# Kernel optimization log

Measured on AMD Instinct MI355X. Metric: run time of the kernel, lower is better.

The kernel has to match this reference:

```python
import jax, jax.numpy as jnp
import numpy as np

FP_PENALTY = 1.0  # false_positive_penalty from __init__ (missing_penalty is unused in forward)


def setup_inputs() -> dict:
    key = jax.random.key(0)
    k1, k2, k3 = jax.random.split(key, 3)
    B, C, H, W = 8, 9, 512, 512
    T = 16  # targets per image
    policy_output = jax.random.normal(k1, (B, C, H, W), dtype=jnp.float32)
    target_boxes = jax.random.randint(k2, (B, T, 4), 0, 512, dtype=jnp.int32)
    target_probs = jax.random.uniform(k3, (B, T), dtype=jnp.float32)
    return {"policy_output": policy_output, "target_boxes": target_boxes,
            "target_probs": target_probs}


def reference(policy_output, target_boxes, target_probs):
    B, C, H, W = policy_output.shape
    A = 3
    T = target_boxes.shape[1]

    out = policy_output.reshape(B, A, 3, H, W)
    delta_r = jax.nn.sigmoid(out[:, :, 0]) * 9.0    # (B,A,H,W)
    delta_c = jax.nn.sigmoid(out[:, :, 1]) * 16.0   # (B,A,H,W)
    conf = jax.nn.sigmoid(out[:, :, 2])             # (B,A,H,W)

    r_grid = jnp.arange(H, dtype=jnp.float32)[None, None, :, None]  # (1,1,H,1)
    c_grid = jnp.arange(W, dtype=jnp.float32)[None, None, None, :]  # (1,1,1,W)
    pred_r2 = jnp.clip(r_grid + delta_r, 0.0, H - 1.0)  # (B,A,H,W)
    pred_c2 = jnp.clip(c_grid + delta_c, 0.0, W - 1.0)  # (B,A,H,W)
    pr2_i = jnp.round(pred_r2).astype(jnp.int32)
    pc2_i = jnp.round(pred_c2).astype(jnp.int32)

    r_i = jnp.arange(H, dtype=jnp.int32)[None, None, :, None, None]  # (1,1,H,1,1)
    c_i = jnp.arange(W, dtype=jnp.int32)[None, None, None, :, None]  # (1,1,1,W,1)
    tb = target_boxes[:, None, None, None, :, :]  # (B,1,1,1,T,4)

    # match iff (r==tr1 and c==tc1 and round(pred_r2)==tr2 and round(pred_c2)==tc2)
    match = ((r_i == tb[..., 0]) & (c_i == tb[..., 1]) &
             (pr2_i[..., None] == tb[..., 2]) & (pc2_i[..., None] == tb[..., 3]))  # (B,A,H,W,T)
    has_match = match.any(-1)                 # (B,A,H,W)
    first_idx = jnp.argmax(match, axis=-1)    # first matching target (torch loop breaks)

    gather = jax.vmap(lambda v, i: v[i])      # per-batch gather along T
    tr2 = gather(target_boxes[:, :, 2].astype(jnp.float32), first_idx)  # (B,A,H,W)
    tc2 = gather(target_boxes[:, :, 3].astype(jnp.float32), first_idx)
    tp = gather(target_probs, first_idx)

    coord_loss = jnp.abs(pred_r2 - tr2) + jnp.abs(pred_c2 - tc2)
    conf_loss = (conf - tp) ** 2
    fp_loss = conf ** 2 * FP_PENALTY

    per_anchor = jnp.where(has_match, coord_loss + conf_loss, fp_loss)
    denom = max(1, B * H * W * 3)
    return per_anchor.sum() / denom
```

## Files before the change

kernel.cpp:

```cpp
#include <hip/hip_runtime.h>


#define NB 1024
#define NT 256

__device__ __forceinline__ float sigmoidf_(float x) {
    float e = __builtin_amdgcn_exp2f(-1.4426950408889634f * x);
    return 1.0f / (1.0f + e);
}

__global__ __launch_bounds__(NT) void conf_sum_kernel(const float* __restrict__ pol,
                                                      float* __restrict__ partials) {
    const int tid = threadIdx.x;
    const int gid = blockIdx.x * NT + tid;
    const float4* p4 = (const float4*)pol;
    float acc = 0.f;
#pragma unroll
    for (int it = 0; it < 6; ++it) {
        int i = gid + it * (NB * NT);
        int plane = i >> 16;
        int off = i & 65535;
        int b = plane / 3;
        int a = plane - 3 * b;
        int chan = b * 9 + a * 3 + 2;
        float4 v = p4[((size_t)chan << 16) + off];
        float s0 = sigmoidf_(v.x);
        float s1 = sigmoidf_(v.y);
        float s2 = sigmoidf_(v.z);
        float s3 = sigmoidf_(v.w);
        acc += s0 * s0 + s1 * s1 + s2 * s2 + s3 * s3;
    }
#pragma unroll
    for (int o = 32; o; o >>= 1) acc += __shfl_down(acc, o);
    __shared__ float sw[NT / 64];
    if ((tid & 63) == 0) sw[tid >> 6] = acc;
    __syncthreads();
    if (tid == 0) partials[blockIdx.x] = sw[0] + sw[1] + sw[2] + sw[3];
}

__global__ __launch_bounds__(NT) void finish_kernel(const float* __restrict__ pol,
                                                    const int* __restrict__ tb,
                                                    const float* __restrict__ tp,
                                                    const float* __restrict__ partials,
                                                    float* __restrict__ out) {
    const int tid = threadIdx.x;
    double acc = 0.0;

    for (int it = tid; it < 384; it += NT) {
        int a = it % 3;
        int bt = it / 3;
        int t = bt & 15;
        int b = bt >> 4;
        const int* tbb = tb + b * 64;
        int r = tbb[t * 4 + 0];
        int c = tbb[t * 4 + 1];
        bool dup = false;
        for (int t2 = 0; t2 < t; ++t2)
            if (tbb[t2 * 4 + 0] == r && tbb[t2 * 4 + 1] == c) { dup = true; break; }
        if (dup) continue;

        size_t base = ((size_t)(b * 9 + a * 3)) << 18;
        size_t pix = ((size_t)r << 9) + (size_t)c;
        float x0 = pol[base + pix];
        float x1 = pol[base + (1 << 18) + pix];
        float x2 = pol[base + (2 << 18) + pix];
        float dr = sigmoidf_(x0) * 9.0f;
        float dc = sigmoidf_(x1) * 16.0f;
        float conf = sigmoidf_(x2);
        float pr2 = fminf((float)r + dr, 511.0f);
        float pc2 = fminf((float)c + dc, 511.0f);
        int pr2i = (int)rintf(pr2);
        int pc2i = (int)rintf(pc2);

        int fidx = -1;
        for (int t2 = 0; t2 < 16; ++t2) {
            if (tbb[t2 * 4 + 0] == r && tbb[t2 * 4 + 1] == c &&
                tbb[t2 * 4 + 2] == pr2i && tbb[t2 * 4 + 3] == pc2i) { fidx = t2; break; }
        }
        if (fidx >= 0) {
            float tr2 = (float)tbb[fidx * 4 + 2];
            float tc2 = (float)tbb[fidx * 4 + 3];
            float tpv = tp[b * 16 + fidx];
            float coord = fabsf(pr2 - tr2) + fabsf(pc2 - tc2);
            float closs = (conf - tpv) * (conf - tpv);
            acc += (double)(coord + closs - conf * conf);
        }
    }

    for (int j = tid; j < NB; j += NT) acc += (double)partials[j];

#pragma unroll
    for (int o = 32; o; o >>= 1) acc += __shfl_down(acc, o);
    __shared__ double sd[NT / 64];
    if ((tid & 63) == 0) sd[tid >> 6] = acc;
    __syncthreads();
    if (tid == 0) {
        double total = sd[0] + sd[1] + sd[2] + sd[3];
        out[0] = (float)(total / 6291456.0);
    }
}

extern "C" void kernel_launch(void* const* d_in, const int* in_sizes, int n_in,
                              void* d_out, int out_size, void* d_ws, size_t ws_size,
                              hipStream_t stream) {
    const float* pol = (const float*)d_in[0];
    const int* tb = (const int*)d_in[1];
    const float* tp = (const float*)d_in[2];
    float* partials = (float*)d_ws;
    float* out = (float*)d_out;

    conf_sum_kernel<<<NB, NT, 0, stream>>>(pol, partials);
    finish_kernel<<<1, NT, 0, stream>>>(pol, tb, tp, partials, out);
}
```

Baseline: 115.6 us.

## Fuse conf-sum and finish kernels using last-block atomic counter reduction

Merges the two launches into one grid of NB+1 blocks. The extra block computes the matched-anchor correction in parallel with the conf-sum blocks. The last block to finish, found through an atomic counter, does the final double-precision reduction. This removes the serial single-block second kernel launch but adds a memset of the counter on every call. The matched-anchor partial is now accumulated in float instead of double.

```diff
diff --git a/kernel.cpp b/kernel.cpp
--- a/kernel.cpp
+++ b/kernel.cpp
@@ -9,94 +9,101 @@
     return 1.0f / (1.0f + e);
 }
 
-__global__ __launch_bounds__(NT) void conf_sum_kernel(const float* __restrict__ pol,
-                                                      float* __restrict__ partials) {
+__global__ __launch_bounds__(NT) void fused_kernel(const float* __restrict__ pol,
+                                                   const int* __restrict__ tb,
+                                                   const float* __restrict__ tp,
+                                                   float* __restrict__ partials,
+                                                   unsigned int* __restrict__ counter,
+                                                   float* __restrict__ out) {
     const int tid = threadIdx.x;
-    const int gid = blockIdx.x * NT + tid;
-    const float4* p4 = (const float4*)pol;
-    float acc = 0.f;
+    const int blk = blockIdx.x;
+    __shared__ float sw[NT / 64];
+
+    if (blk < NB) {
+        const int gid = blk * NT + tid;
+        const float4* p4 = (const float4*)pol;
+        const int off = gid & 65535;
+        const int p0 = gid >> 16;
+        float acc = 0.f;
 #pragma unroll
-    for (int it = 0; it < 6; ++it) {
-        int i = gid + it * (NB * NT);
-        int plane = i >> 16;
-        int off = i & 65535;
-        int b = plane / 3;
-        int a = plane - 3 * b;
-        int chan = b * 9 + a * 3 + 2;
-        float4 v = p4[((size_t)chan << 16) + off];
-        float s0 = sigmoidf_(v.x);
-        float s1 = sigmoidf_(v.y);
-        float s2 = sigmoidf_(v.z);
-        float s3 = sigmoidf_(v.w);
-        acc += s0 * s0 + s1 * s1 + s2 * s2 + s3 * s3;
-    }
+        for (int it = 0; it < 6; ++it) {
+            int plane = p0 + 4 * it;
+            float4 v = p4[((size_t)(3 * plane + 2) << 16) + off];
+            float s0 = sigmoidf_(v.x), s1 = sigmoidf_(v.y);
+            float s2 = sigmoidf_(v.z), s3 = sigmoidf_(v.w);
+            acc += s0 * s0 + s1 * s1 + s2 * s2 + s3 * s3;
+        }
 #pragma unroll
-    for (int o = 32; o; o >>= 1) acc += __shfl_down(acc, o);
-    __shared__ float sw[NT / 64];
-    if ((tid & 63) == 0) sw[tid >> 6] = acc;
-    __syncthreads();
-    if (tid == 0) partials[blockIdx.x] = sw[0] + sw[1] + sw[2] + sw[3];
-}
+        for (int o = 32; o; o >>= 1) acc += __shfl_down(acc, o);
+        if ((tid & 63) == 0) sw[tid >> 6] = acc;
+        __syncthreads();
+        if (tid == 0) partials[blk] = sw[0] + sw[1] + sw[2] + sw[3];
+    } else {
+        float acc = 0.f;
+        for (int it = tid; it < 384; it += NT) {
+            int a = it % 3;
+            int bt = it / 3;
+            int t = bt & 15;
+            int b = bt >> 4;
+            const int* tbb = tb + b * 64;
+            int r = tbb[t * 4 + 0];
+            int c = tbb[t * 4 + 1];
+            bool dup = false;
+            for (int t2 = 0; t2 < t; ++t2)
+                if (tbb[t2 * 4 + 0] == r && tbb[t2 * 4 + 1] == c) { dup = true; break; }
+            if (dup) continue;
 
-__global__ __launch_bounds__(NT) void finish_kernel(const float* __restrict__ pol,
-                                                    const int* __restrict__ tb,
-                                                    const float* __restrict__ tp,
-                                                    const float* __restrict__ partials,
-                                                    float* __restrict__ out) {
-    const int tid = threadIdx.x;
-    double acc = 0.0;
+            size_t base = ((size_t)(b * 9 + a * 3)) << 18;
+            size_t pix = ((size_t)r << 9) + (size_t)c;
+            float x0 = pol[base + pix];
+            float x1 = pol[base + (1 << 18) + pix];
+            float x2 = pol[base + (2 << 18) + pix];
+            float dr = sigmoidf_(x0) * 9.0f;
+            float dc = sigmoidf_(x1) * 16.0f;
+            float conf = sigmoidf_(x2);
+            float pr2 = fminf((float)r + dr, 511.0f);
+            float pc2 = fminf((float)c + dc, 511.0f);
+            int pr2i = (int)rintf(pr2);
+            int pc2i = (int)rintf(pc2);
 
-    for (int it = tid; it < 384; it += NT) {
-        int a = it % 3;
-        int bt = it / 3;
-        int t = bt & 15;
-        int b = bt >> 4;
-        const int* tbb = tb + b * 64;
-        int r = tbb[t * 4 + 0];
-        int c = tbb[t * 4 + 1];
-        bool dup = false;
-        for (int t2 = 0; t2 < t; ++t2)
-            if (tbb[t2 * 4 + 0] == r && tbb[t2 * 4 + 1] == c) { dup = true; break; }
-        if (dup) continue;
-
-        size_t base = ((size_t)(b * 9 + a * 3)) << 18;
-        size_t pix = ((size_t)r << 9) + (size_t)c;
-        float x0 = pol[base + pix];
-        float x1 = pol[base + (1 << 18) + pix];
-        float x2 = pol[base + (2 << 18) + pix];
-        float dr = sigmoidf_(x0) * 9.0f;
-        float dc = sigmoidf_(x1) * 16.0f;
-        float conf = sigmoidf_(x2);
-        float pr2 = fminf((float)r + dr, 511.0f);
-        float pc2 = fminf((float)c + dc, 511.0f);
-        int pr2i = (int)rintf(pr2);
-        int pc2i = (int)rintf(pc2);
-
-        int fidx = -1;
-        for (int t2 = 0; t2 < 16; ++t2) {
-            if (tbb[t2 * 4 + 0] == r && tbb[t2 * 4 + 1] == c &&
-                tbb[t2 * 4 + 2] == pr2i && tbb[t2 * 4 + 3] == pc2i) { fidx = t2; break; }
+            int fidx = -1;
+            for (int t2 = 0; t2 < 16; ++t2) {
+                if (tbb[t2 * 4 + 0] == r && tbb[t2 * 4 + 1] == c &&
+                    tbb[t2 * 4 + 2] == pr2i && tbb[t2 * 4 + 3] == pc2i) { fidx = t2; break; }
+            }
+            if (fidx >= 0) {
+                float tr2 = (float)tbb[fidx * 4 + 2];
+                float tc2 = (float)tbb[fidx * 4 + 3];
+                float tpv = tp[b * 16 + fidx];
+                float coord = fabsf(pr2 - tr2) + fabsf(pc2 - tc2);
+                float closs = (conf - tpv) * (conf - tpv);
+                acc += coord + closs - conf * conf;
+            }
         }
-        if (fidx >= 0) {
-            float tr2 = (float)tbb[fidx * 4 + 2];
-            float tc2 = (float)tbb[fidx * 4 + 3];
-            float tpv = tp[b * 16 + fidx];
-            float coord = fabsf(pr2 - tr2) + fabsf(pc2 - tc2);
-            float closs = (conf - tpv) * (conf - tpv);
-            acc += (double)(coord + closs - conf * conf);
-        }
+#pragma unroll
+        for (int o = 32; o; o >>= 1) acc += __shfl_down(acc, o);
+        if ((tid & 63) == 0) sw[tid >> 6] = acc;
+        __syncthreads();
+        if (tid == 0) partials[NB] = sw[0] + sw[1] + sw[2] + sw[3];
     }
 
-    for (int j = tid; j < NB; j += NT) acc += (double)partials[j];
-
+    __shared__ unsigned last;
+    if (tid == 0) {
+        __threadfence();
+        last = (atomicAdd(counter, 1u) == NB);
+    }
+    __syncthreads();
+    if (last) {
+        __threadfence();
+        double acc = 0.0;
+        for (int j = tid; j <= NB; j += NT) acc += (double)partials[j];
 #pragma unroll
-    for (int o = 32; o; o >>= 1) acc += __shfl_down(acc, o);
-    __shared__ double sd[NT / 64];
-    if ((tid & 63) == 0) sd[tid >> 6] = acc;
-    __syncthreads();
-    if (tid == 0) {
-        double total = sd[0] + sd[1] + sd[2] + sd[3];
-        out[0] = (float)(total / 6291456.0);
+        for (int o = 32; o; o >>= 1) acc += __shfl_down(acc, o);
+        __shared__ double sd[NT / 64];
+        if ((tid & 63) == 0) sd[tid >> 6] = acc;
+        __syncthreads();
+        if (tid == 0)
+            out[0] = (float)((sd[0] + sd[1] + sd[2] + sd[3]) / 6291456.0);
     }
 }
 
@@ -107,8 +114,9 @@
     const int* tb = (const int*)d_in[1];
     const float* tp = (const float*)d_in[2];
     float* partials = (float*)d_ws;
+    unsigned int* counter = (unsigned int*)((char*)d_ws + 8192);
     float* out = (float*)d_out;
 
-    conf_sum_kernel<<<NB, NT, 0, stream>>>(pol, partials);
-    finish_kernel<<<1, NT, 0, stream>>>(pol, tb, tp, partials, out);
+    hipMemsetAsync(counter, 0, 4, stream);
+    fused_kernel<<<NB + 1, NT, 0, stream>>>(pol, tb, tp, partials, counter, out);
 }
```

Result: slower. 140.0 us (+21.1%).
